# Kernel tuning notes

Measured on AMD Instinct MI355X. Metric: run time of the kernel, lower is better.

The kernel has to match this reference:

```python
import jax, jax.numpy as jnp
import numpy as np

N_DST = 50000
N_SRC = 50000
E = 800000
D = 128
R = 3
H_SEM = 128
NEG_SLOPE = 0.2  # DGL GATConv default


def setup_inputs() -> dict:
    key = jax.random.key(0)
    ks = jax.random.split(key, 40)
    s = 1.0 / np.sqrt(D)
    inp = {
        'dst_feat': jax.random.normal(ks[0], (N_DST, D), jnp.float32),
        'src_feat0': jax.random.normal(ks[1], (N_SRC, D), jnp.float32),
        'src_feat1': jax.random.normal(ks[2], (N_SRC, D), jnp.float32),
        'src_feat2': jax.random.normal(ks[3], (N_SRC, D), jnp.float32),
        'sem_W1': jax.random.normal(ks[4], (D, H_SEM), jnp.float32) * s,
        'sem_b1': jnp.zeros((H_SEM,), jnp.float32),
        'sem_W2': jax.random.normal(ks[5], (H_SEM, 1), jnp.float32) * (1.0 / np.sqrt(H_SEM)),
    }
    for r in range(R):
        inp[f'Wg{r}'] = jax.random.normal(ks[6 + r], (D, D), jnp.float32) * s
        inp[f'al{r}'] = jax.random.normal(ks[9 + r], (D,), jnp.float32) * s
        inp[f'ar{r}'] = jax.random.normal(ks[12 + r], (D,), jnp.float32) * s
        inp[f'bg{r}'] = jnp.zeros((D,), jnp.float32)
        inp[f'src_idx{r}'] = jax.random.randint(ks[15 + r], (E,), 0, N_SRC, jnp.int32)
        inp[f'dst_idx{r}'] = jax.random.randint(ks[18 + r], (E,), 0, N_DST, jnp.int32)
    return inp


def _gat(fs, fd, W, al, ar, b, sidx, didx):
    # DGL GATConv, num_heads=1, bipartite, eval mode (no dropout)
    hs = fs @ W                    # [Ns, D]
    hd = fd @ W                    # [Nd, D]
    el = hs @ al                   # [Ns]
    er = hd @ ar                   # [Nd]
    e = jax.nn.leaky_relu(el[sidx] + er[didx], NEG_SLOPE)  # [E]
    # edge softmax over incoming edges of each dst node
    m = jax.ops.segment_max(e, didx, num_segments=N_DST)
    a = jnp.exp(e - m[didx])
    z = jax.ops.segment_sum(a, didx, num_segments=N_DST)
    alpha = a / z[didx]            # [E]
    out = jax.ops.segment_sum(hs[sidx] * alpha[:, None], didx, num_segments=N_DST)
    return jax.nn.elu(out + b)     # [Nd, D]


def reference(dst_feat, src_feat0, src_feat1, src_feat2,
              Wg0, Wg1, Wg2, al0, al1, al2, ar0, ar1, ar2, bg0, bg1, bg2,
              sem_W1, sem_b1, sem_W2,
              src_idx0, src_idx1, src_idx2, dst_idx0, dst_idx1, dst_idx2):
    z0 = _gat(src_feat0, dst_feat, Wg0, al0, ar0, bg0, src_idx0, dst_idx0)
    z1 = _gat(src_feat1, dst_feat, Wg1, al1, ar1, bg1, src_idx1, dst_idx1)
    z2 = _gat(src_feat2, dst_feat, Wg2, al2, ar2, bg2, src_idx2, dst_idx2)
    z_m = jnp.stack([z0, z1, z2], axis=1)            # [N, R, D]
    h = jnp.tanh(z_m @ sem_W1 + sem_b1) @ sem_W2     # [N, R, 1]
    w = h.mean(axis=0)                               # [R, 1]
    a_w = jax.nn.softmax(w, axis=0)                  # [R, 1]
    z = (z_m * a_w[None, :, :]).sum(axis=1)          # [N, D]
    att_mp = a_w.squeeze()                           # [R]
    return (z, att_mp)
```

## Files before the change

### kernel.cpp

```cpp
#include <hip/hip_runtime.h>
#include <math.h>

#define D_DIM 128
#define N_DST 50000
#define N_SRC 50000
#define NE    800000
#define NEG_SLOPE 0.2f

#define NB        196
#define CAP       4608
#define CHUNK     8192
#define NBLK_REL  98
#define GEMM_BLKS 391
#define GEMM_GRID (3 * GEMM_BLKS)
#define ER_PB     43

typedef unsigned short ushort_t;
using f32x4  = __attribute__((ext_vector_type(4))) float;
using bf16x8 = __attribute__((ext_vector_type(8))) short;

__device__ __forceinline__ ushort_t f2bf(float x) {
    unsigned u = __float_as_uint(x);
    unsigned r = (u + 0x7fffu + ((u >> 16) & 1u)) >> 16;
    return (ushort_t)r;
}
__device__ __forceinline__ float bf2f(ushort_t b) {
    return __uint_as_float(((unsigned)b) << 16);
}
__device__ __forceinline__ float bflo(unsigned u) { return __uint_as_float(u << 16); }
__device__ __forceinline__ float bfhi(unsigned u) { return __uint_as_float(u & 0xffff0000u); }
__device__ __forceinline__ float tanh_fast(float x) {
    float e = __expf(2.f * x);
    return 1.f - 2.f / (e + 1.f);
}

__device__ __forceinline__ void cvt8(float4 f0, float4 f1, bf16x8& hi, bf16x8& lo) {
    float f[8] = {f0.x, f0.y, f0.z, f0.w, f1.x, f1.y, f1.z, f1.w};
    #pragma unroll
    for (int i = 0; i < 8; i++) {
        ushort_t h = f2bf(f[i]);
        hi[i] = (short)h;
        lo[i] = (short)(ushort_t)(__float_as_uint(f[i] - bf2f(h)) >> 16);
    }
}

__global__ __launch_bounds__(256) void vecprep_kernel(
        const float* __restrict__ Wg0, const float* __restrict__ Wg1,
        const float* __restrict__ Wg2,
        const float* __restrict__ ar0, const float* __restrict__ ar1,
        const float* __restrict__ ar2,
        const float* __restrict__ W1,
        float* __restrict__ wv, ushort_t* __restrict__ Wt_g,
        ushort_t* __restrict__ WgT_hi, ushort_t* __restrict__ WgT_lo) {
    int bx = blockIdx.x, tid = threadIdx.x;
    if (bx < 3) {
        if (tid < 128) {
            const float* W  = bx == 0 ? Wg0 : (bx == 1 ? Wg1 : Wg2);
            const float* ar = bx == 0 ? ar0 : (bx == 1 ? ar1 : ar2);
            float sar = 0.f;
            for (int j = 0; j < D_DIM; j++) sar = fmaf(W[tid * D_DIM + j], ar[j], sar);
            wv[bx * D_DIM + tid] = sar;
        }
    } else if (bx < 67) {
        int idx = (bx - 3) * 256 + tid;
        int k = idx >> 7, n = idx & 127;
        Wt_g[n * 128 + k] = f2bf(W1[idx]);
    } else {
        int q = bx - 67;
        int rel = q >> 6;
        int idx = (q & 63) * 256 + tid;
        const float* W = rel == 0 ? Wg0 : (rel == 1 ? Wg1 : Wg2);
        int k = idx >> 7, n = idx & 127;
        float v = W[idx];
        ushort_t hi = f2bf(v);
        float lo = v - bf2f(hi);
        WgT_hi[rel * 16384 + n * 128 + k] = hi;
        WgT_lo[rel * 16384 + n * 128 + k] = f2bf(lo);
    }
}

__global__ __launch_bounds__(256) void bucket_scatter_kernel(
        const int* __restrict__ d0, const int* __restrict__ d1, const int* __restrict__ d2,
        const int* __restrict__ s0, const int* __restrict__ s1, const int* __restrict__ s2,
        int* __restrict__ bucketCur, int2* __restrict__ pairs) {
    __shared__ int cnt[NB], base[NB], cur[NB];
    int bx = blockIdx.x;
    int r = bx / NBLK_REL, blk = bx % NBLK_REL;
    const int* dd = r == 0 ? d0 : (r == 1 ? d1 : d2);
    const int* ss = r == 0 ? s0 : (r == 1 ? s1 : s2);
    int tid = threadIdx.x;
    if (tid < NB) { cnt[tid] = 0; cur[tid] = 0; }
    __syncthreads();
    int e0 = blk * CHUNK, e1 = min(e0 + CHUNK, NE);
    for (int e = e0 + tid; e < e1; e += 256) atomicAdd(&cnt[dd[e] >> 8], 1);
    __syncthreads();
    if (tid < NB) base[tid] = cnt[tid] ? atomicAdd(&bucketCur[r * NB + tid], cnt[tid]) : 0;
    __syncthreads();
    for (int e = e0 + tid; e < e1; e += 256) {
        int d = dd[e], b = d >> 8;
        int rank = atomicAdd(&cur[b], 1);
        pairs[(size_t)(r * NB + b) * CAP + base[b] + rank] = make_int2(ss[e], d);
    }
}

__global__ __launch_bounds__(256) void csr_kernel(
        const int2* __restrict__ pairs, const int* __restrict__ bucketCur,
        int* __restrict__ offs, int* __restrict__ cnts, int* __restrict__ perm) {
    __shared__ int hist[256], sc[256], cur[256];
    int bx = blockIdx.x;
    int r = bx / NB, b = bx % NB;
    int tid = threadIdx.x;
    int nE = bucketCur[r * NB + b];
    size_t region = (size_t)(r * NB + b) * CAP;
    const int2* pr = pairs + region;
    hist[tid] = 0;
    __syncthreads();
    for (int i = tid; i < nE; i += 256) atomicAdd(&hist[pr[i].y & 255], 1);
    __syncthreads();
    int v = hist[tid];
    sc[tid] = v;
    __syncthreads();
    for (int off = 1; off < 256; off <<= 1) {
        int t = tid >= off ? sc[tid - off] : 0;
        __syncthreads();
        sc[tid] += t;
        __syncthreads();
    }
    int excl = sc[tid] - v;
    int dstg = b * 256 + tid;
    if (dstg < N_DST) { offs[r * N_DST + dstg] = (int)region + excl; cnts[r * N_DST + dstg] = v; }
    cur[tid] = excl;
    __syncthreads();
    int* pm = perm + region;
    for (int i = tid; i < nE; i += 256) {
        int2 p = pr[i];
        int rank = atomicAdd(&cur[p.y & 255], 1);
        pm[rank] = p.x;
    }
}

__global__ __launch_bounds__(256) void gemm_er_kernel(
        const float* __restrict__ A0, const float* __restrict__ A1, const float* __restrict__ A2,
        const ushort_t* __restrict__ WgT_hi, const ushort_t* __restrict__ WgT_lo,
        const float* __restrict__ al0, const float* __restrict__ al1, const float* __restrict__ al2,
        const float* __restrict__ dstf, const float* __restrict__ wv,
        ushort_t* __restrict__ hs, float* __restrict__ elv) {
    __shared__ ushort_t wls[4][2304];
    int bx = blockIdx.x;
    int rel = bx / GEMM_BLKS, blk = bx % GEMM_BLKS;
    const float* A  = rel == 0 ? A0 : (rel == 1 ? A1 : A2);
    const float* al = rel == 0 ? al0 : (rel == 1 ? al1 : al2);
    const ushort_t* Bh = WgT_hi + rel * 16384;
    const ushort_t* Bl = WgT_lo + rel * 16384;
    ushort_t* C = hs + (size_t)rel * N_SRC * 128;

    int w = threadIdx.x >> 6, lane = threadIdx.x & 63;
    int quad = lane >> 4, l15 = lane & 15;
    int row0 = blk * 128 + w * 32;

    int gr0 = row0 + l15;      if (gr0 > N_SRC - 1) gr0 = N_SRC - 1;
    int gr1 = row0 + 16 + l15; if (gr1 > N_SRC - 1) gr1 = N_SRC - 1;
    const float* a0p = A + (size_t)gr0 * 128 + quad * 8;
    const float* a1p = A + (size_t)gr1 * 128 + quad * 8;

    float4 abuf[2][2][2];
    abuf[0][0][0] = *(const float4*)(a0p + 0);
    abuf[0][0][1] = *(const float4*)(a0p + 4);
    abuf[0][1][0] = *(const float4*)(a1p + 0);
    abuf[0][1][1] = *(const float4*)(a1p + 4);

    f32x4 acc[2][8] = {};
    #pragma unroll
    for (int kc = 0; kc < 4; kc++) {
        const int par = kc & 1;
        if (kc < 3) {
            int ko = (kc + 1) * 32;
            abuf[par ^ 1][0][0] = *(const float4*)(a0p + ko);
            abuf[par ^ 1][0][1] = *(const float4*)(a0p + ko + 4);
            abuf[par ^ 1][1][0] = *(const float4*)(a1p + ko);
            abuf[par ^ 1][1][1] = *(const float4*)(a1p + ko + 4);
        }
        bf16x8 ah[2], alo[2];
        #pragma unroll
        for (int t = 0; t < 2; t++)
            cvt8(abuf[par][t][0], abuf[par][t][1], ah[t], alo[t]);

        int koff = kc * 32 + quad * 8;
        #pragma unroll
        for (int h2 = 0; h2 < 2; h2++) {
            bf16x8 bhv[4], blv[4];
            #pragma unroll
            for (int n4 = 0; n4 < 4; n4++) {
                int nt = h2 * 4 + n4;
                bhv[n4] = *(const bf16x8*)&Bh[(nt * 16 + l15) * 128 + koff];
                blv[n4] = *(const bf16x8*)&Bl[(nt * 16 + l15) * 128 + koff];
            }
            #pragma unroll
            for (int n4 = 0; n4 < 4; n4++) {
                int nt = h2 * 4 + n4;
                #pragma unroll
                for (int t = 0; t < 2; t++) {
                    acc[t][nt] = __builtin_amdgcn_mfma_f32_16x16x32_bf16(ah[t],  bhv[n4], acc[t][nt], 0, 0, 0);
                    acc[t][nt] = __builtin_amdgcn_mfma_f32_16x16x32_bf16(alo[t], bhv[n4], acc[t][nt], 0, 0, 0);
                    acc[t][nt] = __builtin_amdgcn_mfma_f32_16x16x32_bf16(ah[t],  blv[n4], acc[t][nt], 0, 0, 0);
                }
            }
        }
    }

    float alv[8];
    #pragma unroll
    for (int nt = 0; nt < 8; nt++) alv[nt] = al[nt * 16 + l15];
    #pragma unroll
    for (int t = 0; t < 2; t++) {
        float part[4] = {0.f, 0.f, 0.f, 0.f};
        #pragma unroll
        for (int nt = 0; nt < 8; nt++)
            #pragma unroll
            for (int i = 0; i < 4; i++)
                part[i] = fmaf(acc[t][nt][i], alv[nt], part[i]);
        #pragma unroll
        for (int msk = 1; msk < 16; msk <<= 1)
            #pragma unroll
            for (int i = 0; i < 4; i++) part[i] += __shfl_xor(part[i], msk);
        if (l15 == 0) {
            #pragma unroll
            for (int i = 0; i < 4; i++) {
                int gr = row0 + t * 16 + quad * 4 + i;
                if (gr < N_SRC) elv[rel * N_DST + gr] = part[i];
            }
        }
    }

    ushort_t* Csh = wls[w];
    #pragma unroll
    for (int h = 0; h < 2; h++) {
        __asm__ __volatile__("" ::: "memory");
        #pragma unroll
        for (int t = 0; t < 2; t++)
            #pragma unroll
            for (int ntl = 0; ntl < 4; ntl++) {
                int nt = h * 4 + ntl;
                #pragma unroll
                for (int i = 0; i < 4; i++)
                    Csh[(t * 16 + quad * 4 + i) * 72 + ntl * 16 + l15] = f2bf(acc[t][nt][i]);
            }
        __asm__ __volatile__("" ::: "memory");
        int r2 = lane >> 1, cb = (lane & 1) * 32;
        int gr = row0 + r2;
        if (gr < N_SRC) {
            ushort_t* dst = C + (size_t)gr * 128 + h * 64 + cb;
            #pragma unroll
            for (int k2 = 0; k2 < 4; k2++) {
                uint4 v = *(const uint4*)&Csh[r2 * 72 + cb + k2 * 8];
                *(uint4*)(dst + k2 * 8) = v;
            }
        }
    }

    int base = bx * ER_PB;
    if (base < N_DST) {
        int rend = min(base + ER_PB, N_DST);
        float wl0 = wv[lane],       wh0 = wv[lane + 64];
        float wl1 = wv[128 + lane], wh1 = wv[128 + lane + 64];
        float wl2 = wv[256 + lane], wh2 = wv[256 + lane + 64];
        float m0[11], m1[11];
        #pragma unroll
        for (int j = 0; j < 11; j++) {
            int r = base + w + 4 * j;
            int rr = r < rend ? r : base;
            m0[j] = dstf[(size_t)rr * 128 + lane];
            m1[j] = dstf[(size_t)rr * 128 + lane + 64];
        }
        #pragma unroll
        for (int j = 0; j < 11; j++) {
            int r = base + w + 4 * j;
            if (r < rend) {
                float p0 = fmaf(m0[j], wl0, m1[j] * wh0);
                float p1 = fmaf(m0[j], wl1, m1[j] * wh1);
                float p2 = fmaf(m0[j], wl2, m1[j] * wh2);
                #pragma unroll
                for (int off = 32; off > 0; off >>= 1) {
                    p0 += __shfl_down(p0, off);
                    p1 += __shfl_down(p1, off);
                    p2 += __shfl_down(p2, off);
                }
                if (lane == 0) {
                    elv[3 * N_DST + r] = p0;
                    elv[4 * N_DST + r] = p1;
                    elv[5 * N_DST + r] = p2;
                }
            }
        }
    }
}

__global__ __launch_bounds__(256) void aggregate_kernel(
        const ushort_t* __restrict__ hs, const float* __restrict__ elv,
        const int* __restrict__ perm, const int* __restrict__ offs,
        const int* __restrict__ cnts,
        const float* __restrict__ bg0, const float* __restrict__ bg1,
        const float* __restrict__ bg2, float* __restrict__ zm) {
    __shared__ int2 ew[4][128];
    int wave = threadIdx.x >> 6, lane = threadIdx.x & 63;
    int bx  = blockIdx.x;
    int rel = bx / 12500;
    int b   = (bx % 12500) * 4 + wave;
    const float* el  = elv + rel * N_DST;
    float erb = elv[(3 + rel) * N_DST + b];
    const float* bg = rel == 0 ? bg0 : (rel == 1 ? bg1 : bg2);
    const ushort_t* hsr = hs + (size_t)rel * N_SRC * 128;
    int o0 = offs[rel * N_DST + b], deg = cnts[rel * N_DST + b];
    float* zout = zm + ((size_t)b * 3 + rel) * 128;

    if (deg <= 128) {
        int i0 = lane, i1 = lane + 64;
        int s0 = 0, s1 = 0;
        float x0 = -INFINITY, x1 = -INFINITY;
        if (i0 < deg) { s0 = perm[o0 + i0]; float x = el[s0] + erb; x0 = x >= 0.f ? x : NEG_SLOPE * x; }
        if (i1 < deg) { s1 = perm[o0 + i1]; float x = el[s1] + erb; x1 = x >= 0.f ? x : NEG_SLOPE * x; }
        float m = fmaxf(x0, x1);
        #pragma unroll
        for (int msk = 1; msk < 64; msk <<= 1) m = fmaxf(m, __shfl_xor(m, msk));
        float e0 = (i0 < deg) ? __expf(x0 - m) : 0.f;
        float e1 = (i1 < deg) ? __expf(x1 - m) : 0.f;
        float lsum = e0 + e1;
        #pragma unroll
        for (int msk = 1; msk < 64; msk <<= 1) lsum += __shfl_xor(lsum, msk);
        float invz = deg > 0 ? 1.f / lsum : 0.f;

        ew[wave][i0] = make_int2(s0 * 256, __float_as_int(e0 * invz));
        ew[wave][i1] = make_int2(s1 * 256, __float_as_int(e1 * invz));
        __asm__ __volatile__("" ::: "memory");

        int degp = (deg + 7) & ~7;
        const char* base = (const char*)hsr;
        int half = lane >> 5;
        int col8 = (lane & 31) * 8;
        float2 a01 = {0.f, 0.f}, a23 = {0.f, 0.f};
        for (int j = 0; j < degp; j += 8) {
            int2 pA = ew[wave][j + half];
            int2 pB = ew[wave][j + 2 + half];
            int2 pC = ew[wave][j + 4 + half];
            int2 pD = ew[wave][j + 6 + half];
            uint2 hA = *(const uint2*)(base + (unsigned)(pA.x + col8));
            uint2 hB = *(const uint2*)(base + (unsigned)(pB.x + col8));
            uint2 hC = *(const uint2*)(base + (unsigned)(pC.x + col8));
            uint2 hD = *(const uint2*)(base + (unsigned)(pD.x + col8));
            float eA = __int_as_float(pA.y), eB = __int_as_float(pB.y);
            float eC = __int_as_float(pC.y), eD = __int_as_float(pD.y);
            a01.x = fmaf(eA, bflo(hA.x), a01.x); a01.y = fmaf(eA, bfhi(hA.x), a01.y);
            a23.x = fmaf(eA, bflo(hA.y), a23.x); a23.y = fmaf(eA, bfhi(hA.y), a23.y);
            a01.x = fmaf(eB, bflo(hB.x), a01.x); a01.y = fmaf(eB, bfhi(hB.x), a01.y);
            a23.x = fmaf(eB, bflo(hB.y), a23.x); a23.y = fmaf(eB, bfhi(hB.y), a23.y);
            a01.x = fmaf(eC, bflo(hC.x), a01.x); a01.y = fmaf(eC, bfhi(hC.x), a01.y);
            a23.x = fmaf(eC, bflo(hC.y), a23.x); a23.y = fmaf(eC, bfhi(hC.y), a23.y);
            a01.x = fmaf(eD, bflo(hD.x), a01.x); a01.y = fmaf(eD, bfhi(hD.x), a01.y);
            a23.x = fmaf(eD, bflo(hD.y), a23.x); a23.y = fmaf(eD, bfhi(hD.y), a23.y);
        }
        a01.x += __shfl_xor(a01.x, 32);
        a01.y += __shfl_xor(a01.y, 32);
        a23.x += __shfl_xor(a23.x, 32);
        a23.y += __shfl_xor(a23.y, 32);
        if (half == 0) {
            int col4 = (lane & 31) * 4;
            float4 bgv = *(const float4*)&bg[col4];
            float4 z;
            z.x = a01.x + bgv.x;
            z.y = a01.y + bgv.y;
            z.z = a23.x + bgv.z;
            z.w = a23.y + bgv.w;
            z.x = z.x > 0.f ? z.x : expm1f(z.x);
            z.y = z.y > 0.f ? z.y : expm1f(z.y);
            z.z = z.z > 0.f ? z.z : expm1f(z.z);
            z.w = z.w > 0.f ? z.w : expm1f(z.w);
            *(float4*)&zout[col4] = z;
        }
    } else {
        float lmax = -INFINITY;
        for (int i = lane; i < deg; i += 64) {
            int s = perm[o0 + i];
            float x = el[s] + erb;
            x = x >= 0.f ? x : NEG_SLOPE * x;
            lmax = fmaxf(lmax, x);
        }
        #pragma unroll
        for (int msk = 1; msk < 64; msk <<= 1) lmax = fmaxf(lmax, __shfl_xor(lmax, msk));
        float lsum = 0.f;
        for (int i = lane; i < deg; i += 64) {
            int s = perm[o0 + i];
            float x = el[s] + erb;
            x = x >= 0.f ? x : NEG_SLOPE * x;
            lsum += __expf(x - lmax);
        }
        #pragma unroll
        for (int msk = 1; msk < 64; msk <<= 1) lsum += __shfl_xor(lsum, msk);
        float invz = 1.f / lsum;
        float c0 = 0.f, c1 = 0.f;
        int col2 = lane * 2;
        for (int j = 0; j < deg; j++) {
            int s = perm[o0 + j];
            float x = el[s] + erb;
            x = x >= 0.f ? x : NEG_SLOPE * x;
            float e_ = __expf(x - lmax) * invz;
            unsigned hv = *(const unsigned*)(hsr + (size_t)s * 128 + col2);
            c0 = fmaf(e_, bflo(hv), c0);
            c1 = fmaf(e_, bfhi(hv), c1);
        }
        float2 z;
        z.x = c0 + bg[col2];
        z.y = c1 + bg[col2 + 1];
        z.x = z.x > 0.f ? z.x : expm1f(z.x);
        z.y = z.y > 0.f ? z.y : expm1f(z.y);
        *(float2*)&zout[col2] = z;
    }
}

__global__ __launch_bounds__(256) void semantic_kernel(
        const float* __restrict__ zm, const ushort_t* __restrict__ Wt_g,
        const float* __restrict__ b1, const float* __restrict__ W2,
        float* __restrict__ w_sum) {
    __shared__ ushort_t Wt[128 * 136];
    __shared__ float hsum[3];
    const int NROWS = N_DST * 3;
    int tid = threadIdx.x;
    if (tid < 3) hsum[tid] = 0.f;

    #pragma unroll
    for (int i = 0; i < 8; i++) {
        int c = i * 256 + tid;
        int n = c >> 4, c16 = c & 15;
        uint4 t = *(const uint4*)(Wt_g + n * 128 + c16 * 8);
        *(uint4*)&Wt[n * 136 + c16 * 8] = t;
    }
    __syncthreads();

    int w    = tid >> 6, lane = tid & 63;
    int quad = lane >> 4, l15 = lane & 15;
    long row0 = (long)blockIdx.x * 64 + w * 16;
    long rA = row0 + l15; if (rA > NROWS - 1) rA = NROWS - 1;

    f32x4 acc[8] = {};
    #pragma unroll
    for (int kc = 0; kc < 4; kc++) {
        int k0 = kc * 32 + quad * 8;
        const float* src = zm + (size_t)rA * 128 + k0;
        float4 f0 = *(const float4*)src;
        float4 f1 = *(const float4*)(src + 4);
        bf16x8 a;
        a[0] = (short)f2bf(f0.x); a[1] = (short)f2bf(f0.y);
        a[2] = (short)f2bf(f0.z); a[3] = (short)f2bf(f0.w);
        a[4] = (short)f2bf(f1.x); a[5] = (short)f2bf(f1.y);
        a[6] = (short)f2bf(f1.z); a[7] = (short)f2bf(f1.w);
        #pragma unroll
        for (int nt = 0; nt < 8; nt++) {
            int n = nt * 16 + l15;
            bf16x8 bfr = *(const bf16x8*)&Wt[n * 136 + k0];
            acc[nt] = __builtin_amdgcn_mfma_f32_16x16x32_bf16(a, bfr, acc[nt], 0, 0, 0);
        }
    }

    float part[4] = {0.f, 0.f, 0.f, 0.f};
    #pragma unroll
    for (int nt = 0; nt < 8; nt++) {
        int n = nt * 16 + l15;
        float bb = b1[n], ww = W2[n];
        #pragma unroll
        for (int i = 0; i < 4; i++) {
            float t = tanh_fast(acc[nt][i] + bb);
            part[i] = fmaf(t, ww, part[i]);
        }
    }
    #pragma unroll
    for (int msk = 1; msk < 16; msk <<= 1)
        #pragma unroll
        for (int i = 0; i < 4; i++) part[i] += __shfl_xor(part[i], msk);
    if (l15 == 0) {
        #pragma unroll
        for (int i = 0; i < 4; i++) {
            long R = row0 + quad * 4 + i;
            if (R < NROWS) atomicAdd(&hsum[(int)(R % 3)], part[i]);
        }
    }
    __syncthreads();
    if (tid < 3) atomicAdd(&w_sum[tid], hsum[tid]);
}

__global__ void combine_kernel(const float* __restrict__ zm, const float* __restrict__ w_sum,
                               float* __restrict__ out, float* __restrict__ out_att) {
    float w0 = w_sum[0] * (1.f / (float)N_DST);
    float w1 = w_sum[1] * (1.f / (float)N_DST);
    float w2 = w_sum[2] * (1.f / (float)N_DST);
    float m = fmaxf(w0, fmaxf(w1, w2));
    float e0 = __expf(w0 - m), e1 = __expf(w1 - m), e2 = __expf(w2 - m);
    float s = 1.f / (e0 + e1 + e2);
    float a0 = e0 * s, a1 = e1 * s, a2 = e2 * s;
    if (blockIdx.x == 0 && threadIdx.x < 3)
        out_att[threadIdx.x] = threadIdx.x == 0 ? a0 : (threadIdx.x == 1 ? a1 : a2);
    int id4 = blockIdx.x * 256 + threadIdx.x;
    int n  = id4 >> 5;
    int d4 = (id4 & 31) * 4;
    const float4 z0 = *(const float4*)&zm[((size_t)n * 3 + 0) * 128 + d4];
    const float4 z1 = *(const float4*)&zm[((size_t)n * 3 + 1) * 128 + d4];
    const float4 z2 = *(const float4*)&zm[((size_t)n * 3 + 2) * 128 + d4];
    float4 o;
    o.x = a0 * z0.x + a1 * z1.x + a2 * z2.x;
    o.y = a0 * z0.y + a1 * z1.y + a2 * z2.y;
    o.z = a0 * z0.z + a1 * z1.z + a2 * z2.z;
    o.w = a0 * z0.w + a1 * z1.w + a2 * z2.w;
    *(float4*)&out[(size_t)n * 128 + d4] = o;
}

extern "C" void kernel_launch(void* const* d_in, const int* in_sizes, int n_in,
                              void* d_out, int out_size, void* d_ws, size_t ws_size,
                              hipStream_t stream) {
    const float* dstf   = (const float*)d_in[0];
    const float* src0   = (const float*)d_in[1];
    const float* src1   = (const float*)d_in[2];
    const float* src2   = (const float*)d_in[3];
    const float* sem_W1 = (const float*)d_in[4];
    const float* sem_b1 = (const float*)d_in[5];
    const float* sem_W2 = (const float*)d_in[6];
    const float* Wg[3]  = {(const float*)d_in[7],  (const float*)d_in[13], (const float*)d_in[19]};
    const float* al[3]  = {(const float*)d_in[8],  (const float*)d_in[14], (const float*)d_in[20]};
    const float* ar[3]  = {(const float*)d_in[9],  (const float*)d_in[15], (const float*)d_in[21]};
    const float* bg[3]  = {(const float*)d_in[10], (const float*)d_in[16], (const float*)d_in[22]};
    const int*  sidx[3] = {(const int*)d_in[11], (const int*)d_in[17], (const int*)d_in[23]};
    const int*  didx[3] = {(const int*)d_in[12], (const int*)d_in[18], (const int*)d_in[24]};
    float* out = (float*)d_out;

    char* p = (char*)d_ws;
    auto alloc = [&](size_t bytes) -> char* {
        char* q = p; p += (bytes + 255) & ~(size_t)255; return q;
    };
    float*    zm   = (float*)alloc((size_t)N_DST * 3 * 128 * 4);
    ushort_t* hs   = (ushort_t*)alloc((size_t)3 * N_SRC * 128 * 2);
    float*    elv  = (float*)alloc((size_t)6 * N_DST * 4);
    float*    wv   = (float*)alloc((size_t)3 * 128 * 4);
    ushort_t* Wt_g   = (ushort_t*)alloc((size_t)128 * 128 * 2);
    ushort_t* WgT_hi = (ushort_t*)alloc((size_t)3 * 16384 * 2);
    ushort_t* WgT_lo = (ushort_t*)alloc((size_t)3 * 16384 * 2);
    int* cnts = (int*)alloc((size_t)3 * N_DST * 4);
    int* offs = (int*)alloc((size_t)3 * N_DST * 4);
    int* perm = (int*)alloc((size_t)3 * NB * CAP * 4);
    int* zero = (int*)alloc((size_t)(3 * NB + 8) * 4);
    int*   bucketCur = zero;
    float* wsum      = (float*)(zero + 3 * NB);
    int2* pairs = (int2*)zm;

    hipMemsetAsync(zero, 0, (size_t)(3 * NB + 8) * 4, stream);

    vecprep_kernel<<<259, 256, 0, stream>>>(Wg[0], Wg[1], Wg[2], ar[0], ar[1], ar[2],
                                            sem_W1, wv, Wt_g, WgT_hi, WgT_lo);
    bucket_scatter_kernel<<<3 * NBLK_REL, 256, 0, stream>>>(didx[0], didx[1], didx[2],
                                                            sidx[0], sidx[1], sidx[2],
                                                            bucketCur, pairs);
    csr_kernel<<<3 * NB, 256, 0, stream>>>(pairs, bucketCur, offs, cnts, perm);
    gemm_er_kernel<<<GEMM_GRID, 256, 0, stream>>>(src0, src1, src2,
                                                  WgT_hi, WgT_lo,
                                                  al[0], al[1], al[2],
                                                  dstf, wv, hs, elv);
    aggregate_kernel<<<3 * 12500, 256, 0, stream>>>(hs, elv, perm, offs, cnts,
                                                    bg[0], bg[1], bg[2], zm);
    semantic_kernel<<<(3 * N_DST + 63) / 64, 256, 0, stream>>>(zm, Wt_g, sem_b1, sem_W2, wsum);
    combine_kernel<<<6250, 256, 0, stream>>>(zm, wsum, out, out + (size_t)N_DST * 128);
}
```

Baseline: 467.1 us.

## Stage prepacked bf16 weights in LDS and double GEMM block size

The weight matrices are prepacked into an MFMA-fragment layout, with hi and lo parts interleaved. The GEMM kernel now uses 512-thread blocks covering 256 rows and loads that layout into 64KB of shared memory once per block, where it previously read B fragments from global memory. The er rows are prefetched before the epilogue, and the epilogue reuses the shared buffer. The aggregate kernel gains a single-pass path for degree 64 or less that skips the max reduction, and ELU now uses __expf-1 in place of expm1f. This adds precision and overflow risk, since exponentials are taken without subtracting the max and expm1 is less accurate near zero.

```diff
diff --git a/kernel.cpp b/kernel.cpp
--- a/kernel.cpp
+++ b/kernel.cpp
@@ -11,9 +11,9 @@
 #define CAP       4608
 #define CHUNK     8192
 #define NBLK_REL  98
-#define GEMM_BLKS 391
+#define GEMM_BLKS 196
 #define GEMM_GRID (3 * GEMM_BLKS)
-#define ER_PB     43
+#define ER_PB     86
 
 typedef unsigned short ushort_t;
 using f32x4  = __attribute__((ext_vector_type(4))) float;
@@ -51,7 +51,7 @@
         const float* __restrict__ ar2,
         const float* __restrict__ W1,
         float* __restrict__ wv, ushort_t* __restrict__ Wt_g,
-        ushort_t* __restrict__ WgT_hi, ushort_t* __restrict__ WgT_lo) {
+        ushort_t* __restrict__ Bv) {
     int bx = blockIdx.x, tid = threadIdx.x;
     if (bx < 3) {
         if (tid < 128) {
@@ -73,9 +73,15 @@
         int k = idx >> 7, n = idx & 127;
         float v = W[idx];
         ushort_t hi = f2bf(v);
-        float lo = v - bf2f(hi);
-        WgT_hi[rel * 16384 + n * 128 + k] = hi;
-        WgT_lo[rel * 16384 + n * 128 + k] = f2bf(lo);
+        ushort_t lo = f2bf(v - bf2f(hi));
+        int nt = n >> 4, l15 = n & 15;
+        int kc = k >> 5, quad = (k >> 3) & 3, e = k & 7;
+        int h2 = nt >> 2, n4 = nt & 3;
+        int lane = quad * 16 + l15;
+        int fh = kc * 16 + h2 * 8 + n4;
+        ushort_t* dst = Bv + (size_t)rel * 32768;
+        dst[(fh)     * 512 + lane * 8 + e] = hi;
+        dst[(fh + 4) * 512 + lane * 8 + e] = lo;
     }
 }
 
@@ -139,24 +145,30 @@
     }
 }
 
-__global__ __launch_bounds__(256) void gemm_er_kernel(
+__global__ __launch_bounds__(512) void gemm_er_kernel(
         const float* __restrict__ A0, const float* __restrict__ A1, const float* __restrict__ A2,
-        const ushort_t* __restrict__ WgT_hi, const ushort_t* __restrict__ WgT_lo,
+        const ushort_t* __restrict__ Bv,
         const float* __restrict__ al0, const float* __restrict__ al1, const float* __restrict__ al2,
         const float* __restrict__ dstf, const float* __restrict__ wv,
         ushort_t* __restrict__ hs, float* __restrict__ elv) {
-    __shared__ ushort_t wls[4][2304];
+    __shared__ ushort_t Bs[32768];
     int bx = blockIdx.x;
     int rel = bx / GEMM_BLKS, blk = bx % GEMM_BLKS;
     const float* A  = rel == 0 ? A0 : (rel == 1 ? A1 : A2);
     const float* al = rel == 0 ? al0 : (rel == 1 ? al1 : al2);
-    const ushort_t* Bh = WgT_hi + rel * 16384;
-    const ushort_t* Bl = WgT_lo + rel * 16384;
     ushort_t* C = hs + (size_t)rel * N_SRC * 128;
-
-    int w = threadIdx.x >> 6, lane = threadIdx.x & 63;
+    int tid = threadIdx.x;
+
+    {
+        const uint4* src = (const uint4*)(Bv + (size_t)rel * 32768);
+        uint4* dl = (uint4*)Bs;
+        #pragma unroll
+        for (int i = 0; i < 8; i++) dl[tid + i * 512] = src[tid + i * 512];
+    }
+
+    int w = tid >> 6, lane = tid & 63;
     int quad = lane >> 4, l15 = lane & 15;
-    int row0 = blk * 128 + w * 32;
+    int row0 = blk * 256 + w * 32;
 
     int gr0 = row0 + l15;      if (gr0 > N_SRC - 1) gr0 = N_SRC - 1;
     int gr1 = row0 + 16 + l15; if (gr1 > N_SRC - 1) gr1 = N_SRC - 1;
@@ -168,6 +180,8 @@
     abuf[0][0][1] = *(const float4*)(a0p + 4);
     abuf[0][1][0] = *(const float4*)(a1p + 0);
     abuf[0][1][1] = *(const float4*)(a1p + 4);
+
+    __syncthreads();
 
     f32x4 acc[2][8] = {};
     #pragma unroll
@@ -185,24 +199,19 @@
         for (int t = 0; t < 2; t++)
             cvt8(abuf[par][t][0], abuf[par][t][1], ah[t], alo[t]);
 
-        int koff = kc * 32 + quad * 8;
         #pragma unroll
         for (int h2 = 0; h2 < 2; h2++) {
-            bf16x8 bhv[4], blv[4];
             #pragma unroll
             for (int n4 = 0; n4 < 4; n4++) {
-                int nt = h2 * 4 + n4;
-                bhv[n4] = *(const bf16x8*)&Bh[(nt * 16 + l15) * 128 + koff];
-                blv[n4] = *(const bf16x8*)&Bl[(nt * 16 + l15) * 128 + koff];
-            }
-            #pragma unroll
-            for (int n4 = 0; n4 < 4; n4++) {
+                int f = kc * 16 + h2 * 8 + n4;
+                bf16x8 bh = *(const bf16x8*)&Bs[f * 512 + lane * 8];
+                bf16x8 bl = *(const bf16x8*)&Bs[(f + 4) * 512 + lane * 8];
                 int nt = h2 * 4 + n4;
                 #pragma unroll
                 for (int t = 0; t < 2; t++) {
-                    acc[t][nt] = __builtin_amdgcn_mfma_f32_16x16x32_bf16(ah[t],  bhv[n4], acc[t][nt], 0, 0, 0);
-                    acc[t][nt] = __builtin_amdgcn_mfma_f32_16x16x32_bf16(alo[t], bhv[n4], acc[t][nt], 0, 0, 0);
-                    acc[t][nt] = __builtin_amdgcn_mfma_f32_16x16x32_bf16(ah[t],  blv[n4], acc[t][nt], 0, 0, 0);
+                    acc[t][nt] = __builtin_amdgcn_mfma_f32_16x16x32_bf16(ah[t],  bh, acc[t][nt], 0, 0, 0);
+                    acc[t][nt] = __builtin_amdgcn_mfma_f32_16x16x32_bf16(alo[t], bh, acc[t][nt], 0, 0, 0);
+                    acc[t][nt] = __builtin_amdgcn_mfma_f32_16x16x32_bf16(ah[t],  bl, acc[t][nt], 0, 0, 0);
                 }
             }
         }
@@ -232,7 +241,27 @@
         }
     }
 
-    ushort_t* Csh = wls[w];
+    int erbase = bx * ER_PB;
+    float m0[11], m1[11];
+    float wl0 = 0.f, wh0 = 0.f, wl1 = 0.f, wh1 = 0.f, wl2 = 0.f, wh2 = 0.f;
+    int rend = 0;
+    if (erbase < N_DST) {
+        rend = min(erbase + ER_PB, N_DST);
+        wl0 = wv[lane];       wh0 = wv[lane + 64];
+        wl1 = wv[128 + lane]; wh1 = wv[128 + lane + 64];
+        wl2 = wv[256 + lane]; wh2 = wv[256 + lane + 64];
+        #pragma unroll
+        for (int j = 0; j < 11; j++) {
+            int r = erbase + w + 8 * j;
+            int rr = r < rend ? r : erbase;
+            m0[j] = dstf[(size_t)rr * 128 + lane];
+            m1[j] = dstf[(size_t)rr * 128 + lane + 64];
+        }
+    }
+
+    __syncthreads();
+
+    ushort_t* Csh = Bs + w * 2304;
     #pragma unroll
     for (int h = 0; h < 2; h++) {
         __asm__ __volatile__("" ::: "memory");
@@ -258,23 +287,10 @@
         }
     }
 
-    int base = bx * ER_PB;
-    if (base < N_DST) {
-        int rend = min(base + ER_PB, N_DST);
-        float wl0 = wv[lane],       wh0 = wv[lane + 64];
-        float wl1 = wv[128 + lane], wh1 = wv[128 + lane + 64];
-        float wl2 = wv[256 + lane], wh2 = wv[256 + lane + 64];
-        float m0[11], m1[11];
+    if (erbase < N_DST) {
         #pragma unroll
         for (int j = 0; j < 11; j++) {
-            int r = base + w + 4 * j;
-            int rr = r < rend ? r : base;
-            m0[j] = dstf[(size_t)rr * 128 + lane];
-            m1[j] = dstf[(size_t)rr * 128 + lane + 64];
-        }
-        #pragma unroll
-        for (int j = 0; j < 11; j++) {
-            int r = base + w + 4 * j;
+            int r = erbase + w + 8 * j;
             if (r < rend) {
                 float p0 = fmaf(m0[j], wl0, m1[j] * wh0);
                 float p1 = fmaf(m0[j], wl1, m1[j] * wh1);
@@ -314,23 +330,34 @@
     float* zout = zm + ((size_t)b * 3 + rel) * 128;
 
     if (deg <= 128) {
-        int i0 = lane, i1 = lane + 64;
         int s0 = 0, s1 = 0;
-        float x0 = -INFINITY, x1 = -INFINITY;
-        if (i0 < deg) { s0 = perm[o0 + i0]; float x = el[s0] + erb; x0 = x >= 0.f ? x : NEG_SLOPE * x; }
-        if (i1 < deg) { s1 = perm[o0 + i1]; float x = el[s1] + erb; x1 = x >= 0.f ? x : NEG_SLOPE * x; }
-        float m = fmaxf(x0, x1);
-        #pragma unroll
-        for (int msk = 1; msk < 64; msk <<= 1) m = fmaxf(m, __shfl_xor(m, msk));
-        float e0 = (i0 < deg) ? __expf(x0 - m) : 0.f;
-        float e1 = (i1 < deg) ? __expf(x1 - m) : 0.f;
+        float e0 = 0.f, e1 = 0.f;
+        if (deg <= 64) {
+            if (lane < deg) {
+                s0 = perm[o0 + lane];
+                float x = el[s0] + erb;
+                x = x >= 0.f ? x : NEG_SLOPE * x;
+                e0 = __expf(x);
+            }
+        } else {
+            int i0 = lane, i1 = lane + 64;
+            float x0 = -INFINITY, x1 = -INFINITY;
+            if (i0 < deg) { s0 = perm[o0 + i0]; float x = el[s0] + erb; x0 = x >= 0.f ? x : NEG_SLOPE * x; }
+            if (i1 < deg) { s1 = perm[o0 + i1]; float x = el[s1] + erb; x1 = x >= 0.f ? x : NEG_SLOPE * x; }
+            float m = fmaxf(x0, x1);
+            #pragma unroll
+            for (int msk = 1; msk < 64; msk <<= 1) m = fmaxf(m, __shfl_xor(m, msk));
+            e0 = (i0 < deg) ? __expf(x0 - m) : 0.f;
+            e1 = (i1 < deg) ? __expf(x1 - m) : 0.f;
+        }
         float lsum = e0 + e1;
         #pragma unroll
         for (int msk = 1; msk < 64; msk <<= 1) lsum += __shfl_xor(lsum, msk);
         float invz = deg > 0 ? 1.f / lsum : 0.f;
 
-        ew[wave][i0] = make_int2(s0 * 256, __float_as_int(e0 * invz));
-        ew[wave][i1] = make_int2(s1 * 256, __float_as_int(e1 * invz));
+        ew[wave][lane] = make_int2(s0 * 256, __float_as_int(e0 * invz));
+        if (deg > 64)
+            ew[wave][lane + 64] = make_int2(s1 * 256, __float_as_int(e1 * invz));
         __asm__ __volatile__("" ::: "memory");
 
         int degp = (deg + 7) & ~7;
@@ -370,10 +397,10 @@
             z.y = a01.y + bgv.y;
             z.z = a23.x + bgv.z;
             z.w = a23.y + bgv.w;
-            z.x = z.x > 0.f ? z.x : expm1f(z.x);
-            z.y = z.y > 0.f ? z.y : expm1f(z.y);
-            z.z = z.z > 0.f ? z.z : expm1f(z.z);
-            z.w = z.w > 0.f ? z.w : expm1f(z.w);
+            z.x = z.x > 0.f ? z.x : __expf(z.x) - 1.f;
+            z.y = z.y > 0.f ? z.y : __expf(z.y) - 1.f;
+            z.z = z.z > 0.f ? z.z : __expf(z.z) - 1.f;
+            z.w = z.w > 0.f ? z.w : __expf(z.w) - 1.f;
             *(float4*)&zout[col4] = z;
         }
     } else {
@@ -410,8 +437,8 @@
         float2 z;
         z.x = c0 + bg[col2];
         z.y = c1 + bg[col2 + 1];
-        z.x = z.x > 0.f ? z.x : expm1f(z.x);
-        z.y = z.y > 0.f ? z.y : expm1f(z.y);
+        z.x = z.x > 0.f ? z.x : __expf(z.x) - 1.f;
+        z.y = z.y > 0.f ? z.y : __expf(z.y) - 1.f;
         *(float2*)&zout[col2] = z;
     }
 }
@@ -537,9 +564,8 @@
     ushort_t* hs   = (ushort_t*)alloc((size_t)3 * N_SRC * 128 * 2);
     float*    elv  = (float*)alloc((size_t)6 * N_DST * 4);
     float*    wv   = (float*)alloc((size_t)3 * 128 * 4);
-    ushort_t* Wt_g   = (ushort_t*)alloc((size_t)128 * 128 * 2);
-    ushort_t* WgT_hi = (ushort_t*)alloc((size_t)3 * 16384 * 2);
-    ushort_t* WgT_lo = (ushort_t*)alloc((size_t)3 * 16384 * 2);
+    ushort_t* Wt_g = (ushort_t*)alloc((size_t)128 * 128 * 2);
+    ushort_t* Bv   = (ushort_t*)alloc((size_t)3 * 32768 * 2);
     int* cnts = (int*)alloc((size_t)3 * N_DST * 4);
     int* offs = (int*)alloc((size_t)3 * N_DST * 4);
     int* perm = (int*)alloc((size_t)3 * NB * CAP * 4);
@@ -551,13 +577,12 @@
     hipMemsetAsync(zero, 0, (size_t)(3 * NB + 8) * 4, stream);
 
     vecprep_kernel<<<259, 256, 0, stream>>>(Wg[0], Wg[1], Wg[2], ar[0], ar[1], ar[2],
-                                            sem_W1, wv, Wt_g, WgT_hi, WgT_lo);
+                                            sem_W1, wv, Wt_g, Bv);
     bucket_scatter_kernel<<<3 * NBLK_REL, 256, 0, stream>>>(didx[0], didx[1], didx[2],
                                                             sidx[0], sidx[1], sidx[2],
                                                             bucketCur, pairs);
     csr_kernel<<<3 * NB, 256, 0, stream>>>(pairs, bucketCur, offs, cnts, perm);
-    gemm_er_kernel<<<GEMM_GRID, 256, 0, stream>>>(src0, src1, src2,
-                                                  WgT_hi, WgT_lo,
+    gemm_er_kernel<<<GEMM_GRID, 512, 0, stream>>>(src0, src1, src2, Bv,
                                                   al[0], al[1], al[2],
                                                   dstf, wv, hs, elv);
     aggregate_kernel<<<3 * 12500, 256, 0, stream>>>(hs, elv, perm, offs, cnts,
```

New measurement: 435.4 us. 6.8% less time.
